# Optimization experiments

Hardware: AMD Instinct MI355X
Metric: run time of the kernel (lower is better)

Reference implementation:

```python
import jax, jax.numpy as jnp
import numpy as np

N = 50000      # n_nodes
E = 600000     # n_edges (avg degree 12)
IN_DIM = 128
HID = 256
OUT = 2


def _glorot(k, fan_in, fan_out):
    s = jnp.sqrt(6.0 / (fan_in + fan_out))
    return jax.random.uniform(k, (fan_in, fan_out), jnp.float32, -s, s)


def setup_inputs() -> dict:
    key = jax.random.key(0)
    ks = jax.random.split(key, 6)
    x = jax.random.normal(ks[0], (N, IN_DIM), jnp.float32)
    edge_index = jax.random.randint(ks[1], (2, E), 0, N, jnp.int32)
    W1 = _glorot(ks[2], IN_DIM, HID)
    b1 = jnp.zeros((HID,), jnp.float32)
    W2 = _glorot(ks[3], HID, HID)
    b2 = jnp.zeros((HID,), jnp.float32)
    Wl = _glorot(ks[4], HID, OUT)
    bl = jnp.zeros((OUT,), jnp.float32)
    return {"x": x, "edge_index": edge_index, "W1": W1, "b1": b1,
            "W2": W2, "b2": b2, "Wl": Wl, "bl": bl}


def _gcn_conv(x, W, b, src, dst, dinv, n):
    # PyG GCNConv: transform, then propagate with symmetric norm + self-loops.
    h = x @ W                                   # [N, F_out]
    norm = (dinv[src] * dinv[dst])[:, None]     # [E, 1]
    agg = jax.ops.segment_sum(h[src] * norm, dst, num_segments=n)
    agg = agg + h * (dinv * dinv)[:, None]      # self-loop term: deg^-1 * h
    return agg + b


def reference(x, edge_index, W1, b1, W2, b2, Wl, bl):
    n = x.shape[0]
    src, dst = edge_index[0], edge_index[1]
    # degree (with self-loop) computed on destination nodes, as in PyG gcn_norm
    deg = jax.ops.segment_sum(jnp.ones((src.shape[0],), jnp.float32), dst,
                              num_segments=n) + 1.0
    dinv = jax.lax.rsqrt(deg)
    h = jax.nn.relu(_gcn_conv(x, W1, b1, src, dst, dinv, n))
    # dropout is identity in eval mode
    h = jax.nn.relu(_gcn_conv(h, W2, b2, src, dst, dinv, n))
    return h @ Wl + bl
```

## Files before the change

kernel.cpp:

```cpp
#include <hip/hip_runtime.h>
#include <hip/hip_bf16.h>
#include <hip/hip_fp16.h>

constexpr int IN_DIM = 128;
constexpr int HID    = 256;

typedef _Float16 f16x8 __attribute__((ext_vector_type(8)));
typedef float    f32x4 __attribute__((ext_vector_type(4)));

__device__ inline void conv_B_elem(const float* B, ushort* Bp, int id) {
    int k  = id >> 6;
    int n4 = (id & 63) * 4;
    float4 v = *(const float4*)(B + (size_t)k * 256 + n4);
    size_t base = (size_t)(k >> 5) * (256 * 32) + (k & 31);
    Bp[base + (size_t)(n4 + 0) * 32] = __half_as_ushort(__float2half(v.x));
    Bp[base + (size_t)(n4 + 1) * 32] = __half_as_ushort(__float2half(v.y));
    Bp[base + (size_t)(n4 + 2) * 32] = __half_as_ushort(__float2half(v.z));
    Bp[base + (size_t)(n4 + 3) * 32] = __half_as_ushort(__float2half(v.w));
}

__global__ void convert_count(const float* __restrict__ W1, ushort* __restrict__ B1p,
                              const float* __restrict__ W2, ushort* __restrict__ B2p,
                              const float* __restrict__ x, ushort* __restrict__ xh,
                              int total4, const int* __restrict__ dst,
                              ushort* __restrict__ rank, int* __restrict__ deg, int e) {
    int id = blockIdx.x * 256 + threadIdx.x;
    constexpr int C1 = IN_DIM * 64;
    constexpr int C2 = C1 + HID * 64;
    if (id < C1) {
        conv_B_elem(W1, B1p, id);
    } else if (id < C2) {
        conv_B_elem(W2, B2p, id - C1);
    } else if (id < C2 + total4) {
        int i = id - C2;
        float4 v = *(const float4*)(x + (size_t)i * 4);
        ushort4 o;
        o.x = __half_as_ushort(__float2half(v.x));
        o.y = __half_as_ushort(__float2half(v.y));
        o.z = __half_as_ushort(__float2half(v.z));
        o.w = __half_as_ushort(__float2half(v.w));
        *(ushort4*)(xh + (size_t)i * 4) = o;
    } else {
        int i = id - (C2 + total4);
        if (i < e) rank[i] = (ushort)atomicAdd(&deg[dst[i]], 1);
    }
}

__global__ __launch_bounds__(256) void scan_partial(const int* __restrict__ deg,
                                                    int* __restrict__ escan,
                                                    int* __restrict__ blocksum,
                                                    float* __restrict__ dinv, int n) {
    __shared__ int lds[256];
    int t = threadIdx.x;
    int i = blockIdx.x * 256 + t;
    int v = (i < n) ? deg[i] : 0;
    if (i < n) dinv[i] = rsqrtf((float)v + 1.0f);
    lds[t] = v;
    __syncthreads();
    for (int off = 1; off < 256; off <<= 1) {
        int a = lds[t];
        int w = (t >= off) ? lds[t - off] : 0;
        __syncthreads();
        lds[t] = a + w;
        __syncthreads();
    }
    if (i < n) escan[i] = lds[t] - v;
    if (t == 255) blocksum[blockIdx.x] = lds[255];
}

__global__ __launch_bounds__(256) void scanrest_scatter(
    const int* __restrict__ escan, const int* __restrict__ bsum, int nb,
    int* __restrict__ rowptr,
    const int* __restrict__ src, const int* __restrict__ dst,
    const ushort* __restrict__ rank, ushort* __restrict__ esrc,
    int n, int e)
{
    __shared__ int incl[256];
    __shared__ int excl[256];
    int t = threadIdx.x;
    int v = (t < nb) ? bsum[t] : 0;
    incl[t] = v;
    __syncthreads();
    for (int off = 1; off < 256; off <<= 1) {
        int a = incl[t];
        int w = (t >= off) ? incl[t - off] : 0;
        __syncthreads();
        incl[t] = a + w;
        __syncthreads();
    }
    excl[t] = incl[t] - v;
    __syncthreads();

    int gid0    = blockIdx.x * 256 + t;
    int gstride = gridDim.x * 256;
    for (int i = gid0; i < n; i += gstride)
        rowptr[i] = escan[i] + excl[i >> 8];
    if (blockIdx.x == 0 && t == 0) rowptr[n] = incl[nb - 1];
    for (int i = gid0; i < e; i += gstride) {
        int d = dst[i];
        esrc[escan[d] + excl[d >> 8] + (int)rank[i]] = (ushort)src[i];
    }
}

template <int K>
__global__ __launch_bounds__(256) void aggregate_p(const ushort* __restrict__ h,
                                                   const int* __restrict__ rowptr,
                                                   const ushort* __restrict__ esrc,
                                                   const float* __restrict__ dinv,
                                                   ushort* __restrict__ Pp,
                                                   int n, int Mp) {
    constexpr int VH = K / 64;
    int wid  = (blockIdx.x * 256 + threadIdx.x) >> 6;
    int lane = threadIdx.x & 63;
    if (wid >= n) return;
    float di = dinv[wid];
    float acc[VH];
    {
        const ushort* row = h + (size_t)wid * K + lane * VH;
        if constexpr (VH == 4) {
            uint2 u = *(const uint2*)row;
            float2 fa = __half22float2(*(__half2*)&u.x);
            float2 fb = __half22float2(*(__half2*)&u.y);
            acc[0] = fa.x * di; acc[1] = fa.y * di; acc[2] = fb.x * di; acc[3] = fb.y * di;
        } else {
            uint u = *(const uint*)row;
            float2 fa = __half22float2(*(__half2*)&u);
            acc[0] = fa.x * di; acc[1] = fa.y * di;
        }
    }
    int beg = rowptr[wid], fin = rowptr[wid + 1];
    for (int b = beg; b < fin; b += 64) {
        int cnt = fin - b;
        if (cnt > 64) cnt = 64;
        int   sv = (lane < cnt) ? (int)esrc[b + lane] : 0;
        float wv = (lane < cnt) ? dinv[sv] : 0.f;
        int t = 0;
        for (; t + 8 <= cnt; t += 8) {
            float wr[8];
            if constexpr (VH == 4) {
                uint2 u[8];
#pragma unroll
                for (int k = 0; k < 8; k++) {
                    int s = __shfl(sv, t + k);
                    wr[k] = __shfl(wv, t + k);
                    u[k] = *(const uint2*)(h + (size_t)s * K + lane * VH);
                }
#pragma unroll
                for (int k = 0; k < 8; k++) {
                    float2 fa = __half22float2(*(__half2*)&u[k].x);
                    float2 fb = __half22float2(*(__half2*)&u[k].y);
                    acc[0] += fa.x * wr[k]; acc[1] += fa.y * wr[k];
                    acc[2] += fb.x * wr[k]; acc[3] += fb.y * wr[k];
                }
            } else {
                uint u[8];
#pragma unroll
                for (int k = 0; k < 8; k++) {
                    int s = __shfl(sv, t + k);
                    wr[k] = __shfl(wv, t + k);
                    u[k] = *(const uint*)(h + (size_t)s * K + lane * VH);
                }
#pragma unroll
                for (int k = 0; k < 8; k++) {
                    float2 fa = __half22float2(*(__half2*)&u[k]);
                    acc[0] += fa.x * wr[k]; acc[1] += fa.y * wr[k];
                }
            }
        }
        for (; t + 4 <= cnt; t += 4) {
            float wr[4];
            if constexpr (VH == 4) {
                uint2 u[4];
#pragma unroll
                for (int k = 0; k < 4; k++) {
                    int s = __shfl(sv, t + k);
                    wr[k] = __shfl(wv, t + k);
                    u[k] = *(const uint2*)(h + (size_t)s * K + lane * VH);
                }
#pragma unroll
                for (int k = 0; k < 4; k++) {
                    float2 fa = __half22float2(*(__half2*)&u[k].x);
                    float2 fb = __half22float2(*(__half2*)&u[k].y);
                    acc[0] += fa.x * wr[k]; acc[1] += fa.y * wr[k];
                    acc[2] += fb.x * wr[k]; acc[3] += fb.y * wr[k];
                }
            } else {
                uint u[4];
#pragma unroll
                for (int k = 0; k < 4; k++) {
                    int s = __shfl(sv, t + k);
                    wr[k] = __shfl(wv, t + k);
                    u[k] = *(const uint*)(h + (size_t)s * K + lane * VH);
                }
#pragma unroll
                for (int k = 0; k < 4; k++) {
                    float2 fa = __half22float2(*(__half2*)&u[k]);
                    acc[0] += fa.x * wr[k]; acc[1] += fa.y * wr[k];
                }
            }
        }
        for (; t < cnt; t++) {
            int   s = __shfl(sv, t);
            float w = __shfl(wv, t);
            const ushort* r = h + (size_t)s * K + lane * VH;
            if constexpr (VH == 4) {
                uint2 u = *(const uint2*)r;
                float2 fa = __half22float2(*(__half2*)&u.x);
                float2 fb = __half22float2(*(__half2*)&u.y);
                acc[0] += fa.x * w; acc[1] += fa.y * w;
                acc[2] += fb.x * w; acc[3] += fb.y * w;
            } else {
                uint u = *(const uint*)r;
                float2 fa = __half22float2(*(__half2*)&u);
                acc[0] += fa.x * w; acc[1] += fa.y * w;
            }
        }
    }
#pragma unroll
    for (int j = 0; j < VH; j++) acc[j] *= di;

    int kglob = lane * VH;
    int chunk = kglob >> 5;
    int inner = kglob & 31;
    size_t base = (size_t)chunk * Mp * 32 + (size_t)wid * 32 + inner;
    if constexpr (VH == 4) {
        __half2 p0 = __floats2half2_rn(acc[0], acc[1]);
        __half2 p1 = __floats2half2_rn(acc[2], acc[3]);
        *(uint2*)&Pp[base] = make_uint2(*(uint*)&p0, *(uint*)&p1);
    } else {
        __half2 p0 = __floats2half2_rn(acc[0], acc[1]);
        *(uint*)&Pp[base] = *(uint*)&p0;
    }
}

template <int K, int MODE>
__global__ __launch_bounds__(256, (MODE == 1) ? 2 : 1)
void gemm_p(const ushort* __restrict__ Ap, const ushort* __restrict__ Bp,
            const float* __restrict__ bias, ushort* __restrict__ C16,
            const float* __restrict__ Wl, const float* __restrict__ bl,
            float* __restrict__ out, int M, int Mp, int ntiles) {
    constexpr int NC   = K / 32;
    constexpr int NBUF = (MODE == 1) ? 2 : 1;
    __shared__ ushort Bsm[NC * 8192];
    __shared__ ushort Asm[NBUF][NC * 1024];

    int tid  = threadIdx.x;
    int w    = tid >> 6;
    int lane = tid & 63;
    int l15  = lane & 15;
    int quad = lane >> 4;

    for (int j = w; j < NC * 16; j += 4) {
        const ushort* g = Bp + (size_t)j * 512;
        __builtin_amdgcn_global_load_lds(
            (const __attribute__((address_space(1))) uint*)(g + (size_t)lane * 8),
            (__attribute__((address_space(3))) uint*)(Bsm + j * 512), 16, 0, 0);
    }

    auto stageA = [&](ushort* dl, int t) {
        int row0 = t * 32;
        for (int j = w; j < NC * 2; j += 4) {
            int c = j >> 1, sub = j & 1;
            const ushort* g = Ap + (size_t)c * Mp * 32 + (size_t)(row0 + sub * 16) * 32;
            __builtin_amdgcn_global_load_lds(
                (const __attribute__((address_space(1))) uint*)(g + (size_t)lane * 8),
                (__attribute__((address_space(3))) uint*)(dl + c * 1024 + sub * 512),
                16, 0, 0);
        }
    };

    float bj[4];
#pragma unroll
    for (int j = 0; j < 4; j++) bj[j] = bias[w * 64 + j * 16 + l15];
    float wl0[4], wl1[4];
    if constexpr (MODE == 2) {
#pragma unroll
        for (int j = 0; j < 4; j++) {
            int cj = w * 64 + j * 16 + l15;
            float2 wv = *(const float2*)(Wl + cj * 2);
            wl0[j] = wv.x; wl1[j] = wv.y;
        }
    }

    int cur = 0;
    if ((int)blockIdx.x < ntiles) stageA(Asm[0], blockIdx.x);

    for (int t = blockIdx.x; t < ntiles; t += gridDim.x) {
        __syncthreads();
        if constexpr (MODE == 1) {
            if (t + (int)gridDim.x < ntiles) stageA(Asm[cur ^ 1], t + gridDim.x);
        }
        f32x4 acc[2][4] = {};
#pragma unroll
        for (int c = 0; c < NC; c++) {
            f16x8 fa[2], fb[4];
#pragma unroll
            for (int i = 0; i < 2; i++) {
                int off = c * 1024 + (i * 16 + l15) * 32 + quad * 8;
                fa[i] = *(const f16x8*)&Asm[cur][off];
            }
#pragma unroll
            for (int j = 0; j < 4; j++) {
                int off = c * 8192 + (w * 64 + j * 16 + l15) * 32 + quad * 8;
                fb[j] = *(const f16x8*)&Bsm[off];
            }
#pragma unroll
            for (int i = 0; i < 2; i++)
#pragma unroll
                for (int j = 0; j < 4; j++)
                    acc[i][j] = __builtin_amdgcn_mfma_f32_16x16x32_f16(fa[i], fb[j], acc[i][j], 0, 0, 0);
        }

        int row0 = t * 32;
        if constexpr (MODE == 1) {
#pragma unroll
            for (int i = 0; i < 2; i++)
#pragma unroll
                for (int reg = 0; reg < 4; reg++) {
                    int r = row0 + i * 16 + quad * 4 + reg;
                    if (r < M) {
                        ushort* cp = C16 + (size_t)r * 256 + w * 64 + l15;
#pragma unroll
                        for (int j = 0; j < 4; j++) {
                            float v = fmaxf(acc[i][j][reg] + bj[j], 0.f);
                            cp[j * 16] = __half_as_ushort(__float2half(v));
                        }
                    }
                }
            cur ^= 1;
        } else {
            __shared__ float part[4][32][2];
#pragma unroll
            for (int i = 0; i < 2; i++)
#pragma unroll
                for (int reg = 0; reg < 4; reg++) {
                    float s0 = 0.f, s1 = 0.f;
#pragma unroll
                    for (int j = 0; j < 4; j++) {
                        float v = fmaxf(acc[i][j][reg] + bj[j], 0.f);
                        s0 += v * wl0[j];
                        s1 += v * wl1[j];
                    }
#pragma unroll
                    for (int off = 1; off < 16; off <<= 1) {
                        s0 += __shfl_xor(s0, off);
                        s1 += __shfl_xor(s1, off);
                    }
                    if (l15 == 0) {
                        int r = i * 16 + quad * 4 + reg;
                        part[w][r][0] = s0;
                        part[w][r][1] = s1;
                    }
                }
            __syncthreads();
            if (t + (int)gridDim.x < ntiles) stageA(Asm[0], t + gridDim.x);
            if (tid < 64) {
                int r = tid >> 1, o = tid & 1;
                int grr = row0 + r;
                if (grr < M) {
                    float s = part[0][r][o] + part[1][r][o] + part[2][r][o] + part[3][r][o] + bl[o];
                    out[(size_t)grr * 2 + o] = s;
                }
            }
        }
    }
}


extern "C" void kernel_launch(void* const* d_in, const int* in_sizes, int n_in,
                              void* d_out, int out_size, void* d_ws, size_t ws_size,
                              hipStream_t stream) {
    const float* x  = (const float*)d_in[0];
    const int*   ei = (const int*)d_in[1];
    const float* W1 = (const float*)d_in[2];
    const float* b1 = (const float*)d_in[3];
    const float* W2 = (const float*)d_in[4];
    const float* b2 = (const float*)d_in[5];
    const float* Wl = (const float*)d_in[6];
    const float* bl = (const float*)d_in[7];
    float* out = (float*)d_out;

    int n = in_sizes[0] / IN_DIM;
    int e = in_sizes[1] / 2;
    const int* src = ei;
    const int* dst = ei + e;

    int gblocks = (n + 31) / 32;
    int Mp = gblocks * 32;

    char* ws = (char*)d_ws;
    size_t off = 0;
    auto alloc = [&](size_t bytes) -> void* {
        void* p = ws + off;
        off += (bytes + 255) & ~(size_t)255;
        return p;
    };
    int*    deg     = (int*)alloc((size_t)n * 4);
    float*  dinv    = (float*)alloc((size_t)n * 4);
    int*    rowptr  = (int*)alloc((size_t)(n + 1) * 4);
    int*    escan   = (int*)alloc((size_t)n * 4);
    int*    bsum    = (int*)alloc(256 * 4);
    ushort* rank    = (ushort*)alloc((size_t)e * 2);
    ushort* esrc    = (ushort*)alloc((size_t)e * 2);
    ushort* xh      = (ushort*)alloc((size_t)n * IN_DIM * 2);
    ushort* h1      = (ushort*)alloc((size_t)n * HID * 2);
    ushort* A1p     = (ushort*)alloc((size_t)Mp * IN_DIM * 2);
    ushort* A2p     = (ushort*)alloc((size_t)Mp * HID * 2);
    ushort* B1p     = (ushort*)alloc((size_t)IN_DIM * 256 * 2);
    ushort* B2p     = (ushort*)alloc((size_t)HID * 256 * 2);

    int nb = (n + 255) / 256;
    int total4 = n * IN_DIM / 4;

    hipMemsetAsync(deg, 0, (size_t)n * 4, stream);

    int citems = IN_DIM * 64 + HID * 64 + total4 + e;
    convert_count<<<(citems + 255) / 256, 256, 0, stream>>>(W1, B1p, W2, B2p, x, xh,
                                                            total4, dst, rank, deg, e);

    scan_partial<<<nb, 256, 0, stream>>>(deg, escan, bsum, dinv, n);

    int sblocks = (e + 255) / 256;
    if (sblocks > 2048) sblocks = 2048;
    scanrest_scatter<<<sblocks, 256, 0, stream>>>(escan, bsum, nb, rowptr,
                                                  src, dst, rank, esrc, n, e);

    aggregate_p<IN_DIM><<<(n + 3) / 4, 256, 0, stream>>>(xh, rowptr, esrc, dinv,
                                                         A1p, n, Mp);
    gemm_p<IN_DIM, 1><<<512, 256, 0, stream>>>(A1p, B1p, b1, h1,
                                               nullptr, nullptr, nullptr,
                                               n, Mp, gblocks);

    aggregate_p<HID><<<(n + 3) / 4, 256, 0, stream>>>(h1, rowptr, esrc, dinv,
                                                      A2p, n, Mp);
    gemm_p<HID, 2><<<256, 256, 0, stream>>>(A2p, B2p, b2, nullptr,
                                            Wl, bl, out, n, Mp, gblocks);
}
```

Measured before the change: 230.3 us.

## Merge degree scan and edge scatter into one decoupled-lookback kernel

Replaces the two-kernel scan (partial block scan, then a rest-scan plus scatter) with one kernel. Blocks take ordered tickets and run a decoupled look-back prefix scan over the degree chunks, writing rowptr directly. All blocks then spin on a global counter before scattering edge sources. This removes one kernel launch and the escan/bsum intermediate arrays, but adds a grid-wide spin barrier and serial look-back chains.

After: 688.2 us. +198.9%, slower.

```diff
diff --git a/kernel.cpp b/kernel.cpp
--- a/kernel.cpp
+++ b/kernel.cpp
@@ -46,59 +46,86 @@
     }
 }
 
-__global__ __launch_bounds__(256) void scan_partial(const int* __restrict__ deg,
-                                                    int* __restrict__ escan,
-                                                    int* __restrict__ blocksum,
-                                                    float* __restrict__ dinv, int n) {
-    __shared__ int lds[256];
-    int t = threadIdx.x;
-    int i = blockIdx.x * 256 + t;
-    int v = (i < n) ? deg[i] : 0;
-    if (i < n) dinv[i] = rsqrtf((float)v + 1.0f);
-    lds[t] = v;
-    __syncthreads();
-    for (int off = 1; off < 256; off <<= 1) {
-        int a = lds[t];
-        int w = (t >= off) ? lds[t - off] : 0;
-        __syncthreads();
-        lds[t] = a + w;
-        __syncthreads();
-    }
-    if (i < n) escan[i] = lds[t] - v;
-    if (t == 255) blocksum[blockIdx.x] = lds[255];
-}
-
-__global__ __launch_bounds__(256) void scanrest_scatter(
-    const int* __restrict__ escan, const int* __restrict__ bsum, int nb,
-    int* __restrict__ rowptr,
+__global__ __launch_bounds__(256) void scan_scatter(
+    const int* __restrict__ deg,
+    int* __restrict__ aux,
+    unsigned long long* __restrict__ desc,
+    int* __restrict__ rowptr, float* __restrict__ dinv,
     const int* __restrict__ src, const int* __restrict__ dst,
     const ushort* __restrict__ rank, ushort* __restrict__ esrc,
-    int n, int e)
+    int n, int e, int nb)
 {
-    __shared__ int incl[256];
-    __shared__ int excl[256];
+    __shared__ int lds[256];
+    __shared__ int sticket;
+    __shared__ int sprefix;
     int t = threadIdx.x;
-    int v = (t < nb) ? bsum[t] : 0;
-    incl[t] = v;
+    if (t == 0) sticket = atomicAdd(&aux[0], 1);
     __syncthreads();
-    for (int off = 1; off < 256; off <<= 1) {
-        int a = incl[t];
-        int w = (t >= off) ? incl[t - off] : 0;
+    int tk = sticket;
+
+    if (tk < nb) {
+        int i = tk * 256 + t;
+        int v = (i < n) ? deg[i] : 0;
+        if (i < n) dinv[i] = rsqrtf((float)v + 1.0f);
+        lds[t] = v;
         __syncthreads();
-        incl[t] = a + w;
+        for (int off = 1; off < 256; off <<= 1) {
+            int a = lds[t];
+            int w = (t >= off) ? lds[t - off] : 0;
+            __syncthreads();
+            lds[t] = a + w;
+            __syncthreads();
+        }
+        int chunk_total = lds[255];
+        if (t == 0) {
+            if (tk == 0) {
+                __hip_atomic_store(&desc[0], (2ull << 32) | (unsigned)chunk_total,
+                                   __ATOMIC_RELEASE, __HIP_MEMORY_SCOPE_AGENT);
+                sprefix = 0;
+            } else {
+                __hip_atomic_store(&desc[tk], (1ull << 32) | (unsigned)chunk_total,
+                                   __ATOMIC_RELEASE, __HIP_MEMORY_SCOPE_AGENT);
+                int pref = 0;
+                int j = tk - 1;
+                while (true) {
+                    unsigned long long dj = __hip_atomic_load(
+                        &desc[j], __ATOMIC_ACQUIRE, __HIP_MEMORY_SCOPE_AGENT);
+                    unsigned st = (unsigned)(dj >> 32);
+                    if (st == 0) continue;
+                    pref += (int)(unsigned)dj;
+                    if (st == 2u) break;
+                    --j;
+                }
+                __hip_atomic_store(&desc[tk],
+                                   (2ull << 32) | (unsigned)(pref + chunk_total),
+                                   __ATOMIC_RELEASE, __HIP_MEMORY_SCOPE_AGENT);
+                sprefix = pref;
+            }
+        }
         __syncthreads();
-    }
-    excl[t] = incl[t] - v;
+        int pref = sprefix;
+        if (i < n) rowptr[i] = pref + lds[t] - v;
+        if (tk == nb - 1 && t == 255) rowptr[n] = pref + chunk_total;
+        __syncthreads();
+        if (t == 0) {
+            __threadfence();
+            atomicAdd(&aux[1], 1);
+        }
+    }
+
+    if (t == 0) {
+        while (__hip_atomic_load(&aux[1], __ATOMIC_ACQUIRE,
+                                 __HIP_MEMORY_SCOPE_AGENT) < nb) {}
+    }
     __syncthreads();
 
     int gid0    = blockIdx.x * 256 + t;
     int gstride = gridDim.x * 256;
-    for (int i = gid0; i < n; i += gstride)
-        rowptr[i] = escan[i] + excl[i >> 8];
-    if (blockIdx.x == 0 && t == 0) rowptr[n] = incl[nb - 1];
     for (int i = gid0; i < e; i += gstride) {
         int d = dst[i];
-        esrc[escan[d] + excl[d >> 8] + (int)rank[i]] = (ushort)src[i];
+        int rp = __hip_atomic_load(&rowptr[d], __ATOMIC_RELAXED,
+                                   __HIP_MEMORY_SCOPE_AGENT);
+        esrc[rp + (int)rank[i]] = (ushort)src[i];
     }
 }
 
@@ -396,10 +423,11 @@
         return p;
     };
     int*    deg     = (int*)alloc((size_t)n * 4);
+    int*    aux     = (int*)alloc(2 * 4);
+    unsigned long long* desc = (unsigned long long*)alloc(256 * 8);
+    size_t  zbytes  = (size_t)((char*)(desc + 256) - (char*)deg);
     float*  dinv    = (float*)alloc((size_t)n * 4);
     int*    rowptr  = (int*)alloc((size_t)(n + 1) * 4);
-    int*    escan   = (int*)alloc((size_t)n * 4);
-    int*    bsum    = (int*)alloc(256 * 4);
     ushort* rank    = (ushort*)alloc((size_t)e * 2);
     ushort* esrc    = (ushort*)alloc((size_t)e * 2);
     ushort* xh      = (ushort*)alloc((size_t)n * IN_DIM * 2);
@@ -412,18 +440,14 @@
     int nb = (n + 255) / 256;
     int total4 = n * IN_DIM / 4;
 
-    hipMemsetAsync(deg, 0, (size_t)n * 4, stream);
+    hipMemsetAsync(deg, 0, zbytes, stream);
 
     int citems = IN_DIM * 64 + HID * 64 + total4 + e;
     convert_count<<<(citems + 255) / 256, 256, 0, stream>>>(W1, B1p, W2, B2p, x, xh,
                                                             total4, dst, rank, deg, e);
 
-    scan_partial<<<nb, 256, 0, stream>>>(deg, escan, bsum, dinv, n);
-
-    int sblocks = (e + 255) / 256;
-    if (sblocks > 2048) sblocks = 2048;
-    scanrest_scatter<<<sblocks, 256, 0, stream>>>(escan, bsum, nb, rowptr,
-                                                  src, dst, rank, esrc, n, e);
+    scan_scatter<<<2048, 256, 0, stream>>>(deg, aux, desc, rowptr, dinv,
+                                           src, dst, rank, esrc, n, e, nb);
 
     aggregate_p<IN_DIM><<<(n + 3) / 4, 256, 0, stream>>>(xh, rowptr, esrc, dinv,
                                                          A1p, n, Mp);
```
